# Optimization experiments

Measured on AMD Instinct MI355X. Metric: run time of the kernel, lower is better.

The kernel has to match this reference:

```python
import jax, jax.numpy as jnp
import numpy as np

N_ATOM = 819200
N_VIR = 65536
F_DIM = 128
N_GRAPHS = 16384


def setup_inputs() -> dict:
    key = jax.random.key(0)
    k0, k1, k2, k3, k4, k5 = jax.random.split(key, 6)
    scale = 1.0 / np.sqrt(F_DIM)
    return {
        "atom_feats": jax.random.normal(k0, (N_ATOM, F_DIM), dtype=jnp.float32),
        "vir_feats": jax.random.normal(k1, (N_VIR, F_DIM), dtype=jnp.float32),
        "W_atom": jax.random.normal(k2, (F_DIM, 1), dtype=jnp.float32) * scale,
        "b_atom": jnp.zeros((1,), dtype=jnp.float32),
        "W_vir": jax.random.normal(k3, (F_DIM, 1), dtype=jnp.float32) * scale,
        "b_vir": jnp.zeros((1,), dtype=jnp.float32),
        "atom_seg": jnp.sort(jax.random.randint(k4, (N_ATOM,), 0, N_GRAPHS, dtype=jnp.int32)),
        "vir_seg": jnp.sort(jax.random.randint(k5, (N_VIR,), 0, N_GRAPHS, dtype=jnp.int32)),
        "num_graphs": N_GRAPHS,
    }


def reference(atom_feats, vir_feats, W_atom, b_atom, W_vir, b_vir, atom_seg, vir_seg, num_graphs):
    # Linear gate (pre-sigmoid logits returned as atom_weights, matching original)
    atom_logits = atom_feats @ W_atom + b_atom            # [N_atom, 1]
    w_atom = jax.nn.sigmoid(atom_logits)                  # [N_atom, 1]
    w_vir = jax.nn.sigmoid(vir_feats @ W_vir + b_vir)     # [N_vir, 1]

    # Weighted ragged segment sums per graph
    h_g_sum_atom = jax.ops.segment_sum(atom_feats * w_atom, atom_seg, num_segments=num_graphs)
    h_g_sum_vir = jax.ops.segment_sum(vir_feats * w_vir, vir_seg, num_segments=num_graphs)
    return h_g_sum_atom, h_g_sum_vir, atom_logits
```

## Files before the change

kernel.cpp:

```cpp
#include <hip/hip_runtime.h>

#define F_DIM 128
#define UNROLL 8

__device__ __forceinline__ void flush_acc(float* dst, const float4& a) {
    atomicAdd(dst + 0, a.x);
    atomicAdd(dst + 1, a.y);
    atomicAdd(dst + 2, a.z);
    atomicAdd(dst + 3, a.w);
}

__global__ __launch_bounds__(256) void fused_gate_segsum(
    const float* __restrict__ atom_feats, const float* __restrict__ vir_feats,
    const float* __restrict__ W_atom, const float* __restrict__ b_atom,
    const float* __restrict__ W_vir, const float* __restrict__ b_vir,
    const int* __restrict__ atom_seg, const int* __restrict__ vir_seg,
    float* __restrict__ out_atom, float* __restrict__ out_vir,
    float* __restrict__ logits,
    int n_atom, int n_vir, int g_atom, int rpg_atom, int rpg_vir)
{
    const int group = (int)((blockIdx.x * blockDim.x + threadIdx.x) >> 5);
    const int lane  = threadIdx.x & 31;

    const float* feats; const float* W; const float* bp; const int* seg;
    float* out; float* lg; int n_rows; int row_start; int rpg;
    if (group < g_atom) {
        feats = atom_feats; W = W_atom; bp = b_atom; seg = atom_seg;
        out = out_atom; lg = logits; n_rows = n_atom; rpg = rpg_atom;
        row_start = group * rpg;
    } else {
        const int g = group - g_atom;
        feats = vir_feats; W = W_vir; bp = b_vir; seg = vir_seg;
        out = out_vir; lg = nullptr; n_rows = n_vir; rpg = rpg_vir;
        row_start = g * rpg;
    }
    if (row_start >= n_rows) return;
    int row_end = row_start + rpg;
    if (row_end > n_rows) row_end = n_rows;

    const float4 w4 = ((const float4*)W)[lane];
    const float bias = *bp;

    float4 acc = make_float4(0.f, 0.f, 0.f, 0.f);
    int cur = seg[row_start];
    float mylog = 0.f;

    int r = row_start;
    for (; r + UNROLL <= row_end; r += UNROLL) {
        float4 v[UNROLL];
        #pragma unroll
        for (int j = 0; j < UNROLL; ++j)
            v[j] = ((const float4*)(feats + (size_t)(r + j) * F_DIM))[lane];
        const int4 sa = *(const int4*)(seg + r);
        const int4 sb = *(const int4*)(seg + r + 4);
        const int s[UNROLL] = {sa.x, sa.y, sa.z, sa.w, sb.x, sb.y, sb.z, sb.w};

        float d[UNROLL];
        #pragma unroll
        for (int j = 0; j < UNROLL; ++j)
            d[j] = v[j].x * w4.x + v[j].y * w4.y + v[j].z * w4.z + v[j].w * w4.w;

        #pragma unroll
        for (int m = 16; m >= 1; m >>= 1) {
            #pragma unroll
            for (int j = 0; j < UNROLL; ++j)
                d[j] += __shfl_xor(d[j], m, 32);
        }

        #pragma unroll
        for (int j = 0; j < UNROLL; ++j) {
            const float logit = d[j] + bias;
            if (lg) {
                if (lane == ((r + j) & 31)) mylog = logit;
            }
            d[j] = 1.0f / (1.0f + __expf(-logit));
        }
        if (lg && (((r + UNROLL - 1) & 31) == 31)) {
            lg[(r + UNROLL - 32) + lane] = mylog;
        }

        #pragma unroll
        for (int j = 0; j < UNROLL; ++j) {
            if (s[j] != cur) {
                flush_acc(out + (size_t)cur * F_DIM + lane * 4, acc);
                acc = make_float4(0.f, 0.f, 0.f, 0.f);
                cur = s[j];
            }
            acc.x += d[j] * v[j].x; acc.y += d[j] * v[j].y;
            acc.z += d[j] * v[j].z; acc.w += d[j] * v[j].w;
        }
    }

    for (; r < row_end; ++r) {
        const int sv = seg[r];
        const float4 v = ((const float4*)(feats + (size_t)r * F_DIM))[lane];
        float dot = v.x * w4.x + v.y * w4.y + v.z * w4.z + v.w * w4.w;
        #pragma unroll
        for (int m = 16; m >= 1; m >>= 1) dot += __shfl_xor(dot, m, 32);
        const float logit = dot + bias;
        if (lg) {
            if (lane == (r & 31)) mylog = logit;
            if ((r & 31) == 31) lg[r - 31 + lane] = mylog;
        }
        const float wgt = 1.0f / (1.0f + __expf(-logit));
        if (sv != cur) {
            flush_acc(out + (size_t)cur * F_DIM + lane * 4, acc);
            acc = make_float4(0.f, 0.f, 0.f, 0.f);
            cur = sv;
        }
        acc.x += wgt * v.x; acc.y += wgt * v.y;
        acc.z += wgt * v.z; acc.w += wgt * v.w;
    }
    flush_acc(out + (size_t)cur * F_DIM + lane * 4, acc);

    if (lg) {
        const int rem = row_end & 31;
        if (rem && lane < rem) {
            lg[(row_end & ~31) + lane] = mylog;
        }
    }
}

extern "C" void kernel_launch(void* const* d_in, const int* in_sizes, int n_in,
                              void* d_out, int out_size, void* d_ws, size_t ws_size,
                              hipStream_t stream) {
    const float* atom_feats = (const float*)d_in[0];
    const float* vir_feats  = (const float*)d_in[1];
    const float* W_atom     = (const float*)d_in[2];
    const float* b_atom     = (const float*)d_in[3];
    const float* W_vir      = (const float*)d_in[4];
    const float* b_vir      = (const float*)d_in[5];
    const int*   atom_seg   = (const int*)d_in[6];
    const int*   vir_seg    = (const int*)d_in[7];

    const int n_atom = in_sizes[0] / F_DIM;
    const int n_vir  = in_sizes[1] / F_DIM;
    const int num_graphs = (out_size - n_atom) / (2 * F_DIM);

    float* out_atom = (float*)d_out;
    float* out_vir  = out_atom + (size_t)num_graphs * F_DIM;
    float* logits   = out_vir  + (size_t)num_graphs * F_DIM;

    hipMemsetAsync(d_out, 0, (size_t)2 * num_graphs * F_DIM * sizeof(float), stream);

    const int RPG_ATOM = 64;
    const int RPG_VIR  = 16;
    const int g_atom = (n_atom + RPG_ATOM - 1) / RPG_ATOM;
    const int g_vir  = (n_vir  + RPG_VIR  - 1) / RPG_VIR;
    const int total_groups = g_atom + g_vir;
    const int block = 256;
    const int grid = (total_groups * 32 + block - 1) / block;

    fused_gate_segsum<<<grid, block, 0, stream>>>(
        atom_feats, vir_feats, W_atom, b_atom, W_vir, b_vir,
        atom_seg, vir_seg, out_atom, out_vir, logits,
        n_atom, n_vir, g_atom, RPG_ATOM, RPG_VIR);
}
```

Measured before the change: 599.5 us.

## Double-buffer row batches with nontemporal loads and fast reciprocal sigmoid

Replaces the 8-row unrolled loop with a software-pipelined loop over two 4-row batches, loading the next batch while the current one is reduced and accumulated. Feature loads become nontemporal, the sigmoid uses a hardware approximate reciprocal, and rows per group double to 128 for atoms and 32 for virtual nodes. The goal is better hiding of memory latency and fewer atomic flushes per segment, at the cost of less parallelism per row range and slightly lower sigmoid precision.

```diff
diff --git a/kernel.cpp b/kernel.cpp
--- a/kernel.cpp
+++ b/kernel.cpp
@@ -1,13 +1,100 @@
 #include <hip/hip_runtime.h>
 
 #define F_DIM 128
-#define UNROLL 8
+
+typedef float fvec4 __attribute__((ext_vector_type(4)));
 
 __device__ __forceinline__ void flush_acc(float* dst, const float4& a) {
     atomicAdd(dst + 0, a.x);
     atomicAdd(dst + 1, a.y);
     atomicAdd(dst + 2, a.z);
     atomicAdd(dst + 3, a.w);
+}
+
+__device__ __forceinline__ float4 nt_load4(const float* p) {
+    fvec4 t = __builtin_nontemporal_load((const fvec4*)p);
+    return make_float4(t.x, t.y, t.z, t.w);
+}
+
+struct Batch {
+    float4 v0, v1, v2, v3;
+    int4 s;
+};
+
+__device__ __forceinline__ void load_batch(Batch& b, const float* __restrict__ feats,
+                                           const int* __restrict__ seg, int r, int lane) {
+    const float* p = feats + (size_t)r * F_DIM + lane * 4;
+    b.v0 = nt_load4(p);
+    b.v1 = nt_load4(p + F_DIM);
+    b.v2 = nt_load4(p + 2 * F_DIM);
+    b.v3 = nt_load4(p + 3 * F_DIM);
+    b.s  = *(const int4*)(seg + r);
+}
+
+__device__ __forceinline__ float sigmoid_fast(float x) {
+    return __builtin_amdgcn_rcpf(1.0f + __expf(-x));
+}
+
+__device__ __forceinline__ void compute_batch(
+    const Batch& b, const float4& w4, float bias, int r, int lane,
+    float4& acc, int& cur, float& mylog,
+    float* __restrict__ out, float* __restrict__ lg)
+{
+    float d0 = b.v0.x * w4.x + b.v0.y * w4.y + b.v0.z * w4.z + b.v0.w * w4.w;
+    float d1 = b.v1.x * w4.x + b.v1.y * w4.y + b.v1.z * w4.z + b.v1.w * w4.w;
+    float d2 = b.v2.x * w4.x + b.v2.y * w4.y + b.v2.z * w4.z + b.v2.w * w4.w;
+    float d3 = b.v3.x * w4.x + b.v3.y * w4.y + b.v3.z * w4.z + b.v3.w * w4.w;
+
+    #pragma unroll
+    for (int m = 16; m >= 1; m >>= 1) {
+        d0 += __shfl_xor(d0, m, 32);
+        d1 += __shfl_xor(d1, m, 32);
+        d2 += __shfl_xor(d2, m, 32);
+        d3 += __shfl_xor(d3, m, 32);
+    }
+
+    const float l0 = d0 + bias;
+    const float l1 = d1 + bias;
+    const float l2 = d2 + bias;
+    const float l3 = d3 + bias;
+
+    if (lg) {
+        if (lane == ((r + 0) & 31)) mylog = l0;
+        if (lane == ((r + 1) & 31)) mylog = l1;
+        if (lane == ((r + 2) & 31)) mylog = l2;
+        if (lane == ((r + 3) & 31)) mylog = l3;
+        if (((r + 3) & 31) == 31) lg[r + 3 - 31 + lane] = mylog;
+    }
+
+    const float g0 = sigmoid_fast(l0);
+    const float g1 = sigmoid_fast(l1);
+    const float g2 = sigmoid_fast(l2);
+    const float g3 = sigmoid_fast(l3);
+
+    if (b.s.x != cur) {
+        flush_acc(out + (size_t)cur * F_DIM + lane * 4, acc);
+        acc = make_float4(0.f, 0.f, 0.f, 0.f);
+        cur = b.s.x;
+    }
+    acc.x += g0 * b.v0.x; acc.y += g0 * b.v0.y; acc.z += g0 * b.v0.z; acc.w += g0 * b.v0.w;
+    if (b.s.y != cur) {
+        flush_acc(out + (size_t)cur * F_DIM + lane * 4, acc);
+        acc = make_float4(0.f, 0.f, 0.f, 0.f);
+        cur = b.s.y;
+    }
+    acc.x += g1 * b.v1.x; acc.y += g1 * b.v1.y; acc.z += g1 * b.v1.z; acc.w += g1 * b.v1.w;
+    if (b.s.z != cur) {
+        flush_acc(out + (size_t)cur * F_DIM + lane * 4, acc);
+        acc = make_float4(0.f, 0.f, 0.f, 0.f);
+        cur = b.s.z;
+    }
+    acc.x += g2 * b.v2.x; acc.y += g2 * b.v2.y; acc.z += g2 * b.v2.z; acc.w += g2 * b.v2.w;
+    if (b.s.w != cur) {
+        flush_acc(out + (size_t)cur * F_DIM + lane * 4, acc);
+        acc = make_float4(0.f, 0.f, 0.f, 0.f);
+        cur = b.s.w;
+    }
+    acc.x += g3 * b.v3.x; acc.y += g3 * b.v3.y; acc.z += g3 * b.v3.z; acc.w += g3 * b.v3.w;
 }
 
 __global__ __launch_bounds__(256) void fused_gate_segsum(
@@ -46,49 +133,21 @@
     float mylog = 0.f;
 
     int r = row_start;
-    for (; r + UNROLL <= row_end; r += UNROLL) {
-        float4 v[UNROLL];
-        #pragma unroll
-        for (int j = 0; j < UNROLL; ++j)
-            v[j] = ((const float4*)(feats + (size_t)(r + j) * F_DIM))[lane];
-        const int4 sa = *(const int4*)(seg + r);
-        const int4 sb = *(const int4*)(seg + r + 4);
-        const int s[UNROLL] = {sa.x, sa.y, sa.z, sa.w, sb.x, sb.y, sb.z, sb.w};
-
-        float d[UNROLL];
-        #pragma unroll
-        for (int j = 0; j < UNROLL; ++j)
-            d[j] = v[j].x * w4.x + v[j].y * w4.y + v[j].z * w4.z + v[j].w * w4.w;
-
-        #pragma unroll
-        for (int m = 16; m >= 1; m >>= 1) {
-            #pragma unroll
-            for (int j = 0; j < UNROLL; ++j)
-                d[j] += __shfl_xor(d[j], m, 32);
-        }
-
-        #pragma unroll
-        for (int j = 0; j < UNROLL; ++j) {
-            const float logit = d[j] + bias;
-            if (lg) {
-                if (lane == ((r + j) & 31)) mylog = logit;
-            }
-            d[j] = 1.0f / (1.0f + __expf(-logit));
-        }
-        if (lg && (((r + UNROLL - 1) & 31) == 31)) {
-            lg[(r + UNROLL - 32) + lane] = mylog;
-        }
-
-        #pragma unroll
-        for (int j = 0; j < UNROLL; ++j) {
-            if (s[j] != cur) {
-                flush_acc(out + (size_t)cur * F_DIM + lane * 4, acc);
-                acc = make_float4(0.f, 0.f, 0.f, 0.f);
-                cur = s[j];
-            }
-            acc.x += d[j] * v[j].x; acc.y += d[j] * v[j].y;
-            acc.z += d[j] * v[j].z; acc.w += d[j] * v[j].w;
-        }
+    const int nfull = (row_end - row_start) >> 2;
+    Batch A, B;
+    if (nfull > 0) load_batch(A, feats, seg, r, lane);
+    int bidx = 0;
+    for (; bidx + 2 <= nfull; bidx += 2) {
+        load_batch(B, feats, seg, r + 4, lane);
+        compute_batch(A, w4, bias, r, lane, acc, cur, mylog, out, lg);
+        if (bidx + 2 < nfull)
+            load_batch(A, feats, seg, r + 8, lane);
+        compute_batch(B, w4, bias, r + 4, lane, acc, cur, mylog, out, lg);
+        r += 8;
+    }
+    if (bidx < nfull) {
+        compute_batch(A, w4, bias, r, lane, acc, cur, mylog, out, lg);
+        r += 4;
     }
 
     for (; r < row_end; ++r) {
@@ -102,7 +161,7 @@
             if (lane == (r & 31)) mylog = logit;
             if ((r & 31) == 31) lg[r - 31 + lane] = mylog;
         }
-        const float wgt = 1.0f / (1.0f + __expf(-logit));
+        const float wgt = sigmoid_fast(logit);
         if (sv != cur) {
             flush_acc(out + (size_t)cur * F_DIM + lane * 4, acc);
             acc = make_float4(0.f, 0.f, 0.f, 0.f);
@@ -141,10 +200,10 @@
     float* out_vir  = out_atom + (size_t)num_graphs * F_DIM;
     float* logits   = out_vir  + (size_t)num_graphs * F_DIM;
 
-    hipMemsetAsync(d_out, 0, (size_t)2 * num_graphs * F_DIM * sizeof(float), stream);
-
-    const int RPG_ATOM = 64;
-    const int RPG_VIR  = 16;
+    (void)hipMemsetAsync(d_out, 0, (size_t)2 * num_graphs * F_DIM * sizeof(float), stream);
+
+    const int RPG_ATOM = 128;
+    const int RPG_VIR  = 32;
     const int g_atom = (n_atom + RPG_ATOM - 1) / RPG_ATOM;
     const int g_vir  = (n_vir  + RPG_VIR  - 1) / RPG_VIR;
     const int total_groups = g_atom + g_vir;
```

New measurement: 579.5 us. 3.3% less time.
